# Performance work log

Hardware: AMD Instinct MI355X
Metric: run time of the kernel (lower is better)

Reference implementation:

```python
import jax, jax.numpy as jnp
import numpy as np

B, T, C, H = 2, 2048, 1024, 16
D = C // H  # head dim = 64

def setup_inputs() -> dict:
    key = jax.random.key(0)
    k1, k2, k3 = jax.random.split(key, 3)
    x = jax.random.normal(k1, (B, T, C), dtype=jnp.float32)
    Wqkv = jax.random.normal(k2, (C, 3 * C), dtype=jnp.float32) * (1.0 / np.sqrt(C))
    bqkv = jnp.zeros((3 * C,), dtype=jnp.float32)
    Wo = jax.random.normal(k3, (C, C), dtype=jnp.float32) * (1.0 / np.sqrt(C))
    bo = jnp.zeros((C,), dtype=jnp.float32)
    return {"x": x, "Wqkv": Wqkv, "bqkv": bqkv, "Wo": Wo, "bo": bo}

def reference(x, Wqkv, bqkv, Wo, bo):
    b, t, c = x.shape
    qkv = x @ Wqkv + bqkv                              # [B,T,3C]
    q, k, v = jnp.split(qkv, 3, axis=-1)
    # [B,T,C] -> [B,H,T,D]
    q = q.reshape(b, t, H, D).transpose(0, 2, 1, 3)
    k = k.reshape(b, t, H, D).transpose(0, 2, 1, 3)
    v = v.reshape(b, t, H, D).transpose(0, 2, 1, 3)
    scores = jnp.einsum('bhqd,bhkd->bhqk', q, k) * (1.0 / np.sqrt(D))
    causal = jnp.tril(jnp.ones((t, t), dtype=bool))
    scores = jnp.where(causal, scores, -jnp.inf)
    probs = jax.nn.softmax(scores, axis=-1)           # dropout p=0 -> identity
    out = jnp.einsum('bhqk,bhkd->bhqd', probs, v)
    out = out.transpose(0, 2, 1, 3).reshape(b, t, c)
    return out @ Wo + bo
```

## Files before the change

kernel.cpp:

```cpp
#include <hip/hip_runtime.h>
#include <hip/hip_bf16.h>

typedef __attribute__((ext_vector_type(8))) short bf16x8;
typedef __attribute__((ext_vector_type(4))) short bf16x4;
typedef __attribute__((ext_vector_type(4))) float f32x4;

static __device__ __forceinline__ __hip_bfloat16 f2b(float f) {
    return __float2bfloat16(f);
}
static __device__ __forceinline__ unsigned pack2(float a, float b) {
    unsigned ua = (unsigned)__bfloat16_as_ushort(__float2bfloat16(a));
    unsigned ub = (unsigned)__bfloat16_as_ushort(__float2bfloat16(b));
    return ua | (ub << 16);
}
static __device__ __forceinline__ float exp2fast(float x) {
    return __builtin_amdgcn_exp2f(x);
}

#define QSCALE 0.1803368801111f

__global__ __launch_bounds__(256) void k_prep(
    const float* __restrict__ x, __hip_bfloat16* __restrict__ xb,
    const float* __restrict__ Wqkv, __hip_bfloat16* __restrict__ WqkvT,
    const float* __restrict__ Wo, __hip_bfloat16* __restrict__ WoT)
{
    const int bx = blockIdx.x;
    if (bx < 2048) {
        int i = bx * 256 + threadIdx.x;
        const int stride = 2048 * 256;
        for (; i < 1048576; i += stride) {
            float4 v = reinterpret_cast<const float4*>(x)[i];
            __hip_bfloat16* o = xb + 4 * (size_t)i;
            o[0] = f2b(v.x); o[1] = f2b(v.y); o[2] = f2b(v.z); o[3] = f2b(v.w);
        }
        return;
    }
    __shared__ float tile[32][33];
    const float* in;
    __hip_bfloat16* outp;
    int R, Cn, c0, r0;
    if (bx < 5120) {
        const int b = bx - 2048;
        in = Wqkv; outp = WqkvT; R = 1024; Cn = 3072;
        c0 = (b % 96) * 32; r0 = (b / 96) * 32;
    } else {
        const int b = bx - 5120;
        in = Wo; outp = WoT; R = 1024; Cn = 1024;
        c0 = (b & 31) * 32; r0 = (b >> 5) * 32;
    }
    const int tx = threadIdx.x & 31, ty = threadIdx.x >> 5;
#pragma unroll
    for (int i = 0; i < 32; i += 8)
        tile[ty + i][tx] = in[(size_t)(r0 + ty + i) * Cn + c0 + tx];
    __syncthreads();
#pragma unroll
    for (int i = 0; i < 32; i += 8)
        outp[(size_t)(c0 + ty + i) * R + r0 + tx] = f2b(tile[tx][ty + i]);
}

#define QK_STAGE(buf, kt)                                                       \
    {                                                                           \
        const int k0_ = (kt) << 5;                                              \
        _Pragma("unroll")                                                       \
        for (int i = 0; i < 2; ++i) {                                           \
            const int idx = i * 256 + tid;                                      \
            const int r_ = idx >> 2;                                            \
            const int j_ = idx & 3;                                             \
            const int js_ = j_ ^ ((r_ >> 1) & 3);                               \
            __builtin_amdgcn_global_load_lds(                                   \
                (const __attribute__((address_space(1))) void*)(A + (size_t)(m0 + r_) * K + k0_ + js_ * 8), \
                (__attribute__((address_space(3))) void*)(&As[buf][r_][j_ * 8]), 16, 0, 0); \
        }                                                                       \
        _Pragma("unroll")                                                       \
        for (int i = 0; i < 2; ++i) {                                           \
            const int idx = i * 256 + tid;                                      \
            const int r_ = idx >> 2;                                            \
            const int j_ = idx & 3;                                             \
            const int js_ = j_ ^ ((r_ >> 1) & 3);                               \
            __builtin_amdgcn_global_load_lds(                                   \
                (const __attribute__((address_space(1))) void*)(Bt + (size_t)(n0 + r_) * K + k0_ + js_ * 8), \
                (__attribute__((address_space(3))) void*)(&Bs[buf][r_][j_ * 8]), 16, 0, 0); \
        }                                                                       \
    }

__global__ __launch_bounds__(256, 3) void k_gemm_qkv(
    const __hip_bfloat16* __restrict__ A,
    const __hip_bfloat16* __restrict__ Bt,
    const float* __restrict__ bias,
    int K,
    __hip_bfloat16* __restrict__ Qb,
    __hip_bfloat16* __restrict__ Kb,
    __hip_bfloat16* __restrict__ Vt)
{
    __shared__ __hip_bfloat16 As[3][128][32];
    __shared__ __hip_bfloat16 Bs[3][128][32];

    const int tid = threadIdx.x;
    const int lane = tid & 63;
    const int wid = tid >> 6;
    const int wm = wid >> 1, wn = wid & 1;
    const int m0 = blockIdx.y * 128, n0 = blockIdx.x * 128;
    const int l15 = lane & 15, lg = lane >> 4;
    const int rchunk = (lg ^ ((l15 >> 1) & 3)) * 8;

    f32x4 acc[4][4] = {};
    const int nt = K >> 5;

    QK_STAGE(0, 0);
    QK_STAGE(1, 1);
    asm volatile("s_waitcnt vmcnt(4)" ::: "memory");
    __builtin_amdgcn_sched_barrier(0);
    __builtin_amdgcn_s_barrier();
    __builtin_amdgcn_sched_barrier(0);

    for (int t = 0; t < nt; ++t) {
        const int cur = t % 3;
        if (t + 2 < nt) {
            const int nxt = (t + 2) % 3;
            QK_STAGE(nxt, t + 2);
        }
        bf16x8 a[4], bb[4];
#pragma unroll
        for (int m = 0; m < 4; ++m)
            a[m] = *(const bf16x8*)&As[cur][wm * 64 + m * 16 + l15][rchunk];
#pragma unroll
        for (int n = 0; n < 4; ++n)
            bb[n] = *(const bf16x8*)&Bs[cur][wn * 64 + n * 16 + l15][rchunk];
        __builtin_amdgcn_s_setprio(1);
#pragma unroll
        for (int m = 0; m < 4; ++m)
#pragma unroll
            for (int n = 0; n < 4; ++n)
                acc[m][n] = __builtin_amdgcn_mfma_f32_16x16x32_bf16(a[m], bb[n], acc[m][n], 0, 0, 0);
        __builtin_amdgcn_s_setprio(0);
        __builtin_amdgcn_sched_barrier(0);
        if (t + 2 < nt)
            asm volatile("s_waitcnt vmcnt(4)" ::: "memory");
        else
            asm volatile("s_waitcnt vmcnt(0)" ::: "memory");
        __builtin_amdgcn_sched_barrier(0);
        __builtin_amdgcn_s_barrier();
        __builtin_amdgcn_sched_barrier(0);
    }

#pragma unroll
    for (int m = 0; m < 4; ++m) {
        const int row = m0 + wm * 64 + m * 16 + lg * 4;
#pragma unroll
        for (int n = 0; n < 4; ++n) {
            const int col = n0 + wn * 64 + n * 16 + l15;
            const float bv = bias[col];
#pragma unroll
            for (int r = 0; r < 4; ++r) {
                const float val = acc[m][n][r] + bv;
                const int rr = row + r;
                const int sec = col >> 10, cw = col & 1023;
                const int hh = cw >> 6, d = cw & 63;
                const int bq = rr >> 11, tt = rr & 2047;
                const int bh = bq * 16 + hh;
                if (sec == 0)
                    Qb[((size_t)bh * 2048 + tt) * 64 + d] = f2b(val * QSCALE);
                else if (sec == 1)
                    Kb[((size_t)bh * 2048 + tt) * 64 + d] = f2b(val);
                else
                    Vt[((size_t)bh * 64 + d) * 2048 + tt] = f2b(val);
            }
        }
    }
}

#define OUT_STAGE(buf, kt)                                                      \
    {                                                                           \
        const int k0_ = (kt) << 5;                                              \
        _Pragma("unroll")                                                       \
        for (int i = 0; i < 2; ++i) {                                           \
            const int idx = i * 256 + tid;                                      \
            const int r_ = idx >> 2;                                            \
            const int j_ = idx & 3;                                             \
            const int js_ = j_ ^ ((r_ >> 1) & 3);                               \
            __builtin_amdgcn_global_load_lds(                                   \
                (const __attribute__((address_space(1))) void*)(A + (size_t)(m0 + r_) * K + k0_ + js_ * 8), \
                (__attribute__((address_space(3))) void*)(&As[buf][r_][j_ * 8]), 16, 0, 0); \
        }                                                                       \
        {                                                                       \
            const int r_ = tid >> 2;                                            \
            const int j_ = tid & 3;                                             \
            const int js_ = j_ ^ ((r_ >> 1) & 3);                               \
            __builtin_amdgcn_global_load_lds(                                   \
                (const __attribute__((address_space(1))) void*)(Bt + (size_t)(n0 + r_) * K + k0_ + js_ * 8), \
                (__attribute__((address_space(3))) void*)(&Bs[buf][r_][j_ * 8]), 16, 0, 0); \
        }                                                                       \
    }

__global__ __launch_bounds__(256, 4) void k_gemm_out(
    const __hip_bfloat16* __restrict__ A,
    const __hip_bfloat16* __restrict__ Bt,
    const float* __restrict__ bias,
    int K, int Nn,
    float* __restrict__ outf)
{
    __shared__ __hip_bfloat16 As[3][128][32];
    __shared__ __hip_bfloat16 Bs[3][64][32];

    const int tid = threadIdx.x;
    const int lane = tid & 63;
    const int wid = tid >> 6;
    const int wm = wid >> 1, wn = wid & 1;
    const int m0 = blockIdx.y * 128, n0 = blockIdx.x * 64;
    const int l15 = lane & 15, lg = lane >> 4;
    const int rchunk = (lg ^ ((l15 >> 1) & 3)) * 8;

    f32x4 acc[4][2] = {};
    const int nt = K >> 5;

    OUT_STAGE(0, 0);
    OUT_STAGE(1, 1);
    asm volatile("s_waitcnt vmcnt(3)" ::: "memory");
    __builtin_amdgcn_sched_barrier(0);
    __builtin_amdgcn_s_barrier();
    __builtin_amdgcn_sched_barrier(0);

    for (int t = 0; t < nt; ++t) {
        const int cur = t % 3;
        if (t + 2 < nt) {
            const int nxt = (t + 2) % 3;
            OUT_STAGE(nxt, t + 2);
        }
        bf16x8 a[4], bb[2];
#pragma unroll
        for (int m = 0; m < 4; ++m)
            a[m] = *(const bf16x8*)&As[cur][wm * 64 + m * 16 + l15][rchunk];
#pragma unroll
        for (int n = 0; n < 2; ++n)
            bb[n] = *(const bf16x8*)&Bs[cur][wn * 32 + n * 16 + l15][rchunk];
        __builtin_amdgcn_s_setprio(1);
#pragma unroll
        for (int m = 0; m < 4; ++m)
#pragma unroll
            for (int n = 0; n < 2; ++n)
                acc[m][n] = __builtin_amdgcn_mfma_f32_16x16x32_bf16(a[m], bb[n], acc[m][n], 0, 0, 0);
        __builtin_amdgcn_s_setprio(0);
        __builtin_amdgcn_sched_barrier(0);
        if (t + 2 < nt)
            asm volatile("s_waitcnt vmcnt(3)" ::: "memory");
        else
            asm volatile("s_waitcnt vmcnt(0)" ::: "memory");
        __builtin_amdgcn_sched_barrier(0);
        __builtin_amdgcn_s_barrier();
        __builtin_amdgcn_sched_barrier(0);
    }

#pragma unroll
    for (int m = 0; m < 4; ++m) {
        const int row = m0 + wm * 64 + m * 16 + lg * 4;
#pragma unroll
        for (int n = 0; n < 2; ++n) {
            const int col = n0 + wn * 32 + n * 16 + l15;
            const float bv = bias[col];
#pragma unroll
            for (int r = 0; r < 4; ++r)
                outf[(size_t)(row + r) * Nn + col] = acc[m][n][r] + bv;
        }
    }
}

#define DEFER_THR 4.0f

#define AT_STAGE(buf, tt)                                                       \
    {                                                                           \
        const int ks_ = (tt) << 6;                                              \
        _Pragma("unroll")                                                       \
        for (int i = 0; i < 2; ++i) {                                           \
            const int idx = i * 256 + tid;                                      \
            const int r_ = idx >> 3;                                            \
            const int j_ = idx & 7;                                             \
            const int js_ = j_ ^ (r_ & 7);                                      \
            __builtin_amdgcn_global_load_lds(                                   \
                (const __attribute__((address_space(1))) void*)(Kbase + (size_t)(ks_ + r_) * 64 + js_ * 8), \
                (__attribute__((address_space(3))) void*)(&Ks[buf][r_][j_ * 8]), 16, 0, 0); \
        }                                                                       \
        _Pragma("unroll")                                                       \
        for (int i = 0; i < 2; ++i) {                                           \
            const int idx = i * 256 + tid;                                      \
            const int r_ = idx >> 3;                                            \
            const int j_ = idx & 7;                                             \
            const int js_ = j_ ^ (r_ & 7);                                      \
            __builtin_amdgcn_global_load_lds(                                   \
                (const __attribute__((address_space(1))) void*)(Vbase + (size_t)r_ * 2048 + ks_ + js_ * 8), \
                (__attribute__((address_space(3))) void*)(&Vs[buf][r_][j_ * 8]), 16, 0, 0); \
        }                                                                       \
    }

#define FULL_STEP_L(BUF)                                                        \
    {                                                                           \
        bf16x8 bk0[4], bk1[4];                                                  \
        _Pragma("unroll")                                                       \
        for (int kf = 0; kf < 4; ++kf) {                                        \
            bk0[kf] = *(const bf16x8*)&Ks[BUF][kf * 16 + l15][(lg ^ kswz) * 8]; \
            bk1[kf] = *(const bf16x8*)&Ks[BUF][kf * 16 + l15][((4 + lg) ^ kswz) * 8]; \
        }                                                                       \
        f32x4 s[4] = {};                                                        \
        __builtin_amdgcn_s_setprio(1);                                          \
        _Pragma("unroll")                                                       \
        for (int kf = 0; kf < 4; ++kf) {                                        \
            s[kf] = __builtin_amdgcn_mfma_f32_16x16x32_bf16(bk0[kf], aq0, s[kf], 0, 0, 0); \
            s[kf] = __builtin_amdgcn_mfma_f32_16x16x32_bf16(bk1[kf], aq1, s[kf], 0, 0, 0); \
        }                                                                       \
        __builtin_amdgcn_s_setprio(0);                                          \
        float px = fmaxf(fmaxf(fmaxf(s[0][0], s[0][1]), fmaxf(s[0][2], s[0][3])), \
                         fmaxf(fmaxf(s[1][0], s[1][1]), fmaxf(s[1][2], s[1][3]))); \
        px = fmaxf(px, fmaxf(fmaxf(fmaxf(s[2][0], s[2][1]), fmaxf(s[2][2], s[2][3])), \
                             fmaxf(fmaxf(s[3][0], s[3][1]), fmaxf(s[3][2], s[3][3])))); \
        px = fmaxf(px, __shfl_xor(px, 16));                                     \
        px = fmaxf(px, __shfl_xor(px, 32));                                     \
        if (__any(px > m0 + DEFER_THR)) {                                       \
            const float mn_ = fmaxf(m0, px);                                    \
            const float al_ = exp2fast(m0 - mn_);                               \
            m0 = mn_; l0 *= al_;                                                \
            _Pragma("unroll")                                                   \
            for (int dc = 0; dc < 4; ++dc)                                      \
                _Pragma("unroll")                                               \
                for (int r = 0; r < 4; ++r) o[dc][r] *= al_;                    \
        }                                                                       \
        float rs_ = 0.f;                                                        \
        _Pragma("unroll")                                                       \
        for (int kf = 0; kf < 4; ++kf) {                                        \
            _Pragma("unroll")                                                   \
            for (int r = 0; r < 4; ++r) {                                       \
                s[kf][r] = exp2fast(s[kf][r] - m0);                             \
                rs_ += s[kf][r];                                                \
            }                                                                   \
            uint2 w_;                                                           \
            w_.x = pack2(s[kf][0], s[kf][1]);                                   \
            w_.y = pack2(s[kf][2], s[kf][3]);                                   \
            *(uint2*)&Pw[l15 * 64 + ((kf * 16 + lg * 4) ^ swz)] = w_;           \
        }                                                                       \
        rs_ += __shfl_xor(rs_, 16);                                             \
        rs_ += __shfl_xor(rs_, 32);                                             \
        l0 += rs_;                                                              \
        _Pragma("unroll")                                                       \
        for (int c2 = 0; c2 < 2; ++c2) {                                        \
            bf16x8 bv[4];                                                       \
            _Pragma("unroll")                                                   \
            for (int dc = 0; dc < 4; ++dc)                                      \
                bv[dc] = *(const bf16x8*)&Vs[BUF][dc * 16 + l15][(((c2 << 2) | lg) ^ kswz) * 8]; \
            const bf16x8 pb = *(const bf16x8*)&Pw[l15 * 64 + ((c2 * 32 + lg * 8) ^ swz)]; \
            __builtin_amdgcn_s_setprio(1);                                      \
            _Pragma("unroll")                                                   \
            for (int dc = 0; dc < 4; ++dc)                                      \
                o[dc] = __builtin_amdgcn_mfma_f32_16x16x32_bf16(bv[dc], pb, o[dc], 0, 0, 0); \
            __builtin_amdgcn_s_setprio(0);                                      \
        }                                                                       \
    }

#define TAIL_STEP_L(BUF)                                                        \
    {                                                                           \
        const int ks_ = nfull * 64;                                             \
        const int qv = qw + l15;                                                \
        bf16x8 bk0[4], bk1[4];                                                  \
        _Pragma("unroll")                                                       \
        for (int kf = 0; kf < 4; ++kf) {                                        \
            bk0[kf] = *(const bf16x8*)&Ks[BUF][kf * 16 + l15][(lg ^ kswz) * 8]; \
            bk1[kf] = *(const bf16x8*)&Ks[BUF][kf * 16 + l15][((4 + lg) ^ kswz) * 8]; \
        }                                                                       \
        f32x4 s[4] = {};                                                        \
        _Pragma("unroll")                                                       \
        for (int kf = 0; kf < 4; ++kf) {                                        \
            if (ks_ + kf * 16 <= qw + 15) {                                     \
                s[kf] = __builtin_amdgcn_mfma_f32_16x16x32_bf16(bk0[kf], aq0, s[kf], 0, 0, 0); \
                s[kf] = __builtin_amdgcn_mfma_f32_16x16x32_bf16(bk1[kf], aq1, s[kf], 0, 0, 0); \
            }                                                                   \
        }                                                                       \
        const int kb = ks_ + lg * 4;                                            \
        _Pragma("unroll")                                                       \
        for (int kf = 0; kf < 4; ++kf)                                          \
            _Pragma("unroll")                                                   \
            for (int r = 0; r < 4; ++r)                                         \
                s[kf][r] = (kb + kf * 16 + r <= qv) ? s[kf][r] : -1e30f;        \
        float mx = fmaxf(fmaxf(fmaxf(s[0][0], s[0][1]), fmaxf(s[0][2], s[0][3])), \
                         fmaxf(fmaxf(s[1][0], s[1][1]), fmaxf(s[1][2], s[1][3]))); \
        mx = fmaxf(mx, fmaxf(fmaxf(fmaxf(s[2][0], s[2][1]), fmaxf(s[2][2], s[2][3])), \
                             fmaxf(fmaxf(s[3][0], s[3][1]), fmaxf(s[3][2], s[3][3])))); \
        mx = fmaxf(mx, __shfl_xor(mx, 16));                                     \
        mx = fmaxf(mx, __shfl_xor(mx, 32));                                     \
        const float mnew = fmaxf(m0, mx);                                       \
        const float al_ = exp2fast(m0 - mnew);                                  \
        m0 = mnew;                                                              \
        float rs_ = 0.f;                                                        \
        _Pragma("unroll")                                                       \
        for (int kf = 0; kf < 4; ++kf)                                          \
            _Pragma("unroll")                                                   \
            for (int r = 0; r < 4; ++r) {                                       \
                s[kf][r] = exp2fast(s[kf][r] - mnew);                           \
                rs_ += s[kf][r];                                                \
            }                                                                   \
        rs_ += __shfl_xor(rs_, 16);                                             \
        rs_ += __shfl_xor(rs_, 32);                                             \
        l0 = l0 * al_ + rs_;                                                    \
        _Pragma("unroll")                                                       \
        for (int dc = 0; dc < 4; ++dc)                                          \
            _Pragma("unroll")                                                   \
            for (int r = 0; r < 4; ++r) o[dc][r] *= al_;                        \
        _Pragma("unroll")                                                       \
        for (int kf = 0; kf < 4; ++kf) {                                        \
            uint2 w_;                                                           \
            w_.x = pack2(s[kf][0], s[kf][1]);                                   \
            w_.y = pack2(s[kf][2], s[kf][3]);                                   \
            *(uint2*)&Pw[l15 * 64 + ((kf * 16 + lg * 4) ^ swz)] = w_;           \
        }                                                                       \
        _Pragma("unroll")                                                       \
        for (int c2 = 0; c2 < 2; ++c2) {                                        \
            if (ks_ + c2 * 32 <= qw + 15) {                                     \
                bf16x8 bv[4];                                                   \
                _Pragma("unroll")                                               \
                for (int dc = 0; dc < 4; ++dc)                                  \
                    bv[dc] = *(const bf16x8*)&Vs[BUF][dc * 16 + l15][(((c2 << 2) | lg) ^ kswz) * 8]; \
                const bf16x8 pb = *(const bf16x8*)&Pw[l15 * 64 + ((c2 * 32 + lg * 8) ^ swz)]; \
                _Pragma("unroll")                                               \
                for (int dc = 0; dc < 4; ++dc)                                  \
                    o[dc] = __builtin_amdgcn_mfma_f32_16x16x32_bf16(bv[dc], pb, o[dc], 0, 0, 0); \
            }                                                                   \
        }                                                                       \
    }

__global__ __launch_bounds__(256, 4) void k_attn(
    const __hip_bfloat16* __restrict__ Qb,
    const __hip_bfloat16* __restrict__ Kb,
    const __hip_bfloat16* __restrict__ Vt,
    __hip_bfloat16* __restrict__ att)
{
    __shared__ __hip_bfloat16 Ks[2][64][64];
    __shared__ __hip_bfloat16 Vs[2][64][64];
    __shared__ __hip_bfloat16 P_lds[4][16 * 64];
    const int tid = threadIdx.x, lane = tid & 63, wid = tid >> 6;
    const int lid = blockIdx.x;
    const int xcd = lid & 7, j = lid >> 3;
    const int bh = xcd * 4 + (j & 3);
    const int v = j >> 2;
    const int tile = (v < 8) ? (31 - v) : ((v < 16) ? (v - 8) : ((v < 24) ? (39 - v) : (v - 16)));
    const int q0 = tile * 64;
    const int qw = q0 + wid * 16;
    const int l15 = lane & 15, lg = lane >> 4;
    const int swz = (l15 & 7) << 3;
    const int kswz = l15 & 7;

    const __hip_bfloat16* Qbase = Qb + (size_t)bh * 2048 * 64;
    const __hip_bfloat16* Kbase = Kb + (size_t)bh * 2048 * 64;
    const __hip_bfloat16* Vbase = Vt + (size_t)bh * 64 * 2048;

    const bf16x8 aq0 = *(const bf16x8*)(Qbase + (size_t)(qw + l15) * 64 + lg * 8);
    const bf16x8 aq1 = *(const bf16x8*)(Qbase + (size_t)(qw + l15) * 64 + 32 + lg * 8);

    f32x4 o[4] = {};
    float m0 = -1e30f, l0 = 0.f;

    const int nfull = qw >> 6;
    const int NT = tile + 1;
    __hip_bfloat16* Pw = &P_lds[wid][0];

    AT_STAGE(0, 0);
    __syncthreads();

    int cur = 0;
    for (int tt = 0; tt < NT; ++tt) {
        if (tt + 1 < NT) AT_STAGE(cur ^ 1, tt + 1);
        if (tt < nfull) {
            FULL_STEP_L(cur);
        } else {
            TAIL_STEP_L(cur);
        }
        __syncthreads();
        cur ^= 1;
    }

    const int bq = bh >> 4, hh = bh & 15;
    const float inv = 1.0f / l0;
    const size_t rowb = ((size_t)(bq * 2048 + qw + l15)) * 1024 + hh * 64;
#pragma unroll
    for (int dc = 0; dc < 4; ++dc) {
        bf16x4 st;
#pragma unroll
        for (int r = 0; r < 4; ++r)
            st[r] = (short)__bfloat16_as_ushort(__float2bfloat16(o[dc][r] * inv));
        *(bf16x4*)(att + rowb + dc * 16 + lg * 4) = st;
    }
}

extern "C" void kernel_launch(void* const* d_in, const int* in_sizes, int n_in,
                              void* d_out, int out_size, void* d_ws, size_t ws_size,
                              hipStream_t stream)
{
    const float* x    = (const float*)d_in[0];
    const float* Wqkv = (const float*)d_in[1];
    const float* bqkv = (const float*)d_in[2];
    const float* Wo   = (const float*)d_in[3];
    const float* bo   = (const float*)d_in[4];
    float* out = (float*)d_out;

    char* ws = (char*)d_ws;
    const size_t MB = 1024 * 1024;
    __hip_bfloat16* xb    = (__hip_bfloat16*)(ws);
    __hip_bfloat16* WqkvT = (__hip_bfloat16*)(ws + 8 * MB);
    __hip_bfloat16* WoT   = (__hip_bfloat16*)(ws + 14 * MB);
    __hip_bfloat16* Qb    = (__hip_bfloat16*)(ws + 16 * MB);
    __hip_bfloat16* Kb    = (__hip_bfloat16*)(ws + 24 * MB);
    __hip_bfloat16* Vt    = (__hip_bfloat16*)(ws + 32 * MB);
    __hip_bfloat16* att   = (__hip_bfloat16*)(ws + 40 * MB);

    k_prep<<<6144, 256, 0, stream>>>(x, xb, Wqkv, WqkvT, Wo, WoT);

    k_gemm_qkv<<<dim3(24, 32), 256, 0, stream>>>(
        xb, WqkvT, bqkv, 1024, Qb, Kb, Vt);

    k_attn<<<1024, 256, 0, stream>>>(Qb, Kb, Vt, att);

    k_gemm_out<<<dim3(16, 32), 256, 0, stream>>>(
        att, WoT, bo, 1024, 1024, out);
}
```

Baseline: 116.1 us.

## Split causal attention KV range across two blocks and merge partial softmax results

Each query tile of the attention kernel is now processed by two blocks. Each block covers half of the causal key range and writes an unnormalized partial output plus its running max and sum, launching 2048 blocks instead of 1024. A new merge kernel rescales the two partials with the softmax statistics and writes the normalized bf16 result. This is meant to even out the causal load imbalance across blocks and raise parallelism. The cost is an extra kernel launch, extra global traffic for the partials (stored in reused workspace regions), and an extra bf16 rounding of the unnormalized partial outputs.

```diff
diff --git a/kernel.cpp b/kernel.cpp
--- a/kernel.cpp
+++ b/kernel.cpp
@@ -15,6 +15,12 @@
 }
 static __device__ __forceinline__ float exp2fast(float x) {
     return __builtin_amdgcn_exp2f(x);
+}
+static __device__ __forceinline__ float b2f(short u) {
+    unsigned ub = ((unsigned)(unsigned short)u) << 16;
+    float f;
+    __builtin_memcpy(&f, &ub, 4);
+    return f;
 }
 
 #define QSCALE 0.1803368801111f
@@ -427,7 +433,9 @@
     const __hip_bfloat16* __restrict__ Qb,
     const __hip_bfloat16* __restrict__ Kb,
     const __hip_bfloat16* __restrict__ Vt,
-    __hip_bfloat16* __restrict__ att)
+    __hip_bfloat16* __restrict__ att,
+    __hip_bfloat16* __restrict__ Po,
+    float* __restrict__ Pml)
 {
     __shared__ __hip_bfloat16 Ks[2][64][64];
     __shared__ __hip_bfloat16 Vs[2][64][64];
@@ -436,8 +444,9 @@
     const int lid = blockIdx.x;
     const int xcd = lid & 7, j = lid >> 3;
     const int bh = xcd * 4 + (j & 3);
-    const int v = j >> 2;
-    const int tile = (v < 8) ? (31 - v) : ((v < 16) ? (v - 8) : ((v < 24) ? (39 - v) : (v - 16)));
+    const int u = j >> 2;
+    const int tile = 31 - (u >> 1);
+    const int half = 1 - (u & 1);
     const int q0 = tile * 64;
     const int qw = q0 + wid * 16;
     const int l15 = lane & 15, lg = lane >> 4;
@@ -455,35 +464,86 @@
     float m0 = -1e30f, l0 = 0.f;
 
     const int nfull = qw >> 6;
-    const int NT = tile + 1;
+    const int nA = tile >> 1;
+    const int kt0 = half ? nA : 0;
+    const int ktEnd = half ? (tile + 1) : nA;
     __hip_bfloat16* Pw = &P_lds[wid][0];
 
-    AT_STAGE(0, 0);
-    __syncthreads();
-
-    int cur = 0;
-    for (int tt = 0; tt < NT; ++tt) {
-        if (tt + 1 < NT) AT_STAGE(cur ^ 1, tt + 1);
-        if (tt < nfull) {
-            FULL_STEP_L(cur);
-        } else {
-            TAIL_STEP_L(cur);
-        }
+    if (ktEnd > kt0) {
+        AT_STAGE(0, kt0);
         __syncthreads();
-        cur ^= 1;
-    }
-
-    const int bq = bh >> 4, hh = bh & 15;
-    const float inv = 1.0f / l0;
-    const size_t rowb = ((size_t)(bq * 2048 + qw + l15)) * 1024 + hh * 64;
-#pragma unroll
-    for (int dc = 0; dc < 4; ++dc) {
-        bf16x4 st;
-#pragma unroll
-        for (int r = 0; r < 4; ++r)
-            st[r] = (short)__bfloat16_as_ushort(__float2bfloat16(o[dc][r] * inv));
-        *(bf16x4*)(att + rowb + dc * 16 + lg * 4) = st;
-    }
+        int cur = 0;
+        for (int tt = kt0; tt < ktEnd; ++tt) {
+            if (tt + 1 < ktEnd) AT_STAGE(cur ^ 1, tt + 1);
+            if (tt < nfull) {
+                FULL_STEP_L(cur);
+            } else {
+                TAIL_STEP_L(cur);
+            }
+            __syncthreads();
+            cur ^= 1;
+        }
+    }
+
+    if (half == 0) {
+        const int bq = bh >> 4, hh = bh & 15;
+        const int qrow = qw + l15;
+        const size_t rowb = ((size_t)(bq * 2048 + qrow)) * 1024 + hh * 64;
+#pragma unroll
+        for (int dc = 0; dc < 4; ++dc) {
+            bf16x4 st;
+#pragma unroll
+            for (int r = 0; r < 4; ++r)
+                st[r] = (short)__bfloat16_as_ushort(__float2bfloat16(o[dc][r]));
+            *(bf16x4*)(att + rowb + dc * 16 + lg * 4) = st;
+        }
+        if (lg == 0) {
+            float2 ml;
+            ml.x = m0;
+            ml.y = l0;
+            ((float2*)Pml)[(size_t)bh * 2048 + qrow] = ml;
+        }
+    } else {
+        const size_t prow = (size_t)bh * 2048 + qw + l15;
+#pragma unroll
+        for (int dc = 0; dc < 4; ++dc) {
+            bf16x4 st;
+#pragma unroll
+            for (int r = 0; r < 4; ++r)
+                st[r] = (short)__bfloat16_as_ushort(__float2bfloat16(o[dc][r]));
+            *(bf16x4*)(Po + prow * 64 + dc * 16 + lg * 4) = st;
+        }
+        if (lg == 0) {
+            float2 ml;
+            ml.x = m0;
+            ml.y = l0;
+            ((float2*)Pml)[65536 + prow] = ml;
+        }
+    }
+}
+
+__global__ __launch_bounds__(256) void k_attn_merge(
+    const __hip_bfloat16* __restrict__ Po,
+    const float* __restrict__ Pml,
+    __hip_bfloat16* __restrict__ att)
+{
+    const int idx = blockIdx.x * 256 + threadIdx.x;
+    const int row = idx >> 3, seg = idx & 7;
+    const float2 mlA = ((const float2*)Pml)[row];
+    const float2 mlB = ((const float2*)Pml)[65536 + row];
+    const float mf = fmaxf(mlA.x, mlB.x);
+    const float aA = exp2fast(mlA.x - mf), aB = exp2fast(mlB.x - mf);
+    const float inv = 1.0f / (mlA.y * aA + mlB.y * aB);
+    const float fA = aA * inv, fB = aB * inv;
+    const int bh = row >> 11, qrow = row & 2047;
+    __hip_bfloat16* dst = att + ((size_t)((bh >> 4) * 2048 + qrow) * 1024 + (bh & 15) * 64 + seg * 8);
+    const bf16x8 oa = *(const bf16x8*)dst;
+    const bf16x8 ob = *(const bf16x8*)(Po + (size_t)row * 64 + seg * 8);
+    bf16x8 st;
+#pragma unroll
+    for (int i = 0; i < 8; ++i)
+        st[i] = (short)__bfloat16_as_ushort(f2b(b2f(oa[i]) * fA + b2f(ob[i]) * fB));
+    *(bf16x8*)dst = st;
 }
 
 extern "C" void kernel_launch(void* const* d_in, const int* in_sizes, int n_in,
@@ -506,13 +566,17 @@
     __hip_bfloat16* Kb    = (__hip_bfloat16*)(ws + 24 * MB);
     __hip_bfloat16* Vt    = (__hip_bfloat16*)(ws + 32 * MB);
     __hip_bfloat16* att   = (__hip_bfloat16*)(ws + 40 * MB);
+    __hip_bfloat16* Po    = (__hip_bfloat16*)(ws);
+    float*          Pml   = (float*)(ws + 8 * MB);
 
     k_prep<<<6144, 256, 0, stream>>>(x, xb, Wqkv, WqkvT, Wo, WoT);
 
     k_gemm_qkv<<<dim3(24, 32), 256, 0, stream>>>(
         xb, WqkvT, bqkv, 1024, Qb, Kb, Vt);
 
-    k_attn<<<1024, 256, 0, stream>>>(Qb, Kb, Vt, att);
+    k_attn<<<2048, 256, 0, stream>>>(Qb, Kb, Vt, att, Po, Pml);
+
+    k_attn_merge<<<2048, 256, 0, stream>>>(Po, Pml, att);
 
     k_gemm_out<<<dim3(16, 32), 256, 0, stream>>>(
         att, WoT, bo, 1024, 1024, out);
```

Measured after the change: 119.3 us. 1.03x slower.
